# Kernel tuning notes

Hardware: AMD Instinct MI355X
Metric: run time of the kernel (lower is better)

## Reference

```python
import jax, jax.numpy as jnp
import numpy as np
import math

B, L, D, H = 4, 1024, 512, 8
TAU = 0.1
LN_EPS = 1e-5


def _attn(xq, xk, xv, wq, bq, wk, bk, wv, bv, wo, bo, energy=None, threshold=None):
    Bq, Lq, Dm = xq.shape
    Dh = Dm // H
    Q = (xq @ wq.T + bq).reshape(Bq, Lq, H, Dh)
    K = (xk @ wk.T + bk).reshape(Bq, -1, H, Dh)
    V = (xv @ wv.T + bv).reshape(Bq, -1, H, Dh)
    sc = jnp.einsum('bqhd,bkhd->bhqk', Q, K) / jnp.sqrt(jnp.float32(Dh))
    if energy is not None:
        # mask keys whose mean |energy| over channels is below threshold
        mask = jnp.abs(energy).mean(-1)[:, None, None, :] > threshold  # (B,1,1,Lk)
        sc = jnp.where(mask, sc, -jnp.inf)
    w = jnp.nan_to_num(jax.nn.softmax(sc, axis=-1))  # nan->0 for fully-masked rows
    o = jnp.einsum('bhqk,bkhd->bqhd', w, V).reshape(Bq, Lq, Dm)
    return o @ wo.T + bo


def _ln(x, w, b):
    m = x.mean(-1, keepdims=True)
    v = x.var(-1, keepdims=True)
    return (x - m) / jnp.sqrt(v + LN_EPS) * w + b


def _mlp(x, w1, b1, w2, b2):
    h = jax.nn.gelu(x @ w1.T + b1, approximate=False)  # torch nn.GELU default = exact
    return h @ w2.T + b2


def setup_inputs():
    key = jax.random.key(0)
    ks = list(jax.random.split(key, 64))

    def nxt():
        return ks.pop(0)

    def w(shape, scale=0.02):
        return jax.random.normal(nxt(), shape, dtype=jnp.float32) * scale

    inp = {
        'LL': jax.random.normal(nxt(), (B, D, L), dtype=jnp.float32),
        'LH': jax.random.normal(nxt(), (B, D, L), dtype=jnp.float32),
        'raw_tau': jnp.float32(math.log(TAU / (1.0 - TAU))),
    }
    for p in ('llA', 'lhA', 'crA'):
        for nm in ('q', 'k', 'v', 'o'):
            inp[f'{p}_w{nm}'] = w((D, D))
            inp[f'{p}_b{nm}'] = jnp.zeros((D,), jnp.float32)
    for p in ('mlp_ll', 'mlp_lh'):
        inp[f'{p}_w1'] = w((4 * D, D))
        inp[f'{p}_b1'] = jnp.zeros((4 * D,), jnp.float32)
        inp[f'{p}_w2'] = w((D, 4 * D))
        inp[f'{p}_b2'] = jnp.zeros((D,), jnp.float32)
    inp['n1_w'] = jnp.ones((D,), jnp.float32)
    inp['n1_b'] = jnp.zeros((D,), jnp.float32)
    inp['n2_w'] = jnp.ones((D,), jnp.float32)
    inp['n2_b'] = jnp.zeros((D,), jnp.float32)
    return inp


def reference(LL, LH, raw_tau,
              llA_wq, llA_bq, llA_wk, llA_bk, llA_wv, llA_bv, llA_wo, llA_bo,
              lhA_wq, lhA_bq, lhA_wk, lhA_bk, lhA_wv, lhA_bv, lhA_wo, lhA_bo,
              crA_wq, crA_bq, crA_wk, crA_bk, crA_wv, crA_bv, crA_wo, crA_bo,
              mlp_ll_w1, mlp_ll_b1, mlp_ll_w2, mlp_ll_b2,
              mlp_lh_w1, mlp_lh_b1, mlp_lh_w2, mlp_lh_b2,
              n1_w, n1_b, n2_w, n2_b):
    tau = jax.nn.sigmoid(raw_tau)
    ll_s = jnp.transpose(LL, (0, 2, 1))  # (B,L,D)
    lh_s = jnp.transpose(LH, (0, 2, 1))
    ll_o = _attn(ll_s, ll_s, ll_s, llA_wq, llA_bq, llA_wk, llA_bk, llA_wv, llA_bv, llA_wo, llA_bo)
    lh_o = _attn(lh_s, lh_s, lh_s, lhA_wq, lhA_bq, lhA_wk, lhA_bk, lhA_wv, lhA_bv, lhA_wo, lhA_bo,
                 energy=lh_s, threshold=tau)
    cr_o = _attn(ll_o, lh_o, lh_o, crA_wq, crA_bq, crA_wk, crA_bk, crA_wv, crA_bv, crA_wo, crA_bo)
    ll_f = _ln(ll_s + ll_o + cr_o, n1_w, n1_b)
    ll_f = _mlp(ll_f, mlp_ll_w1, mlp_ll_b1, mlp_ll_w2, mlp_ll_b2) + ll_f
    lh_f = _ln(lh_s + lh_o, n2_w, n2_b)
    lh_f = _mlp(lh_f, mlp_lh_w1, mlp_lh_b1, mlp_lh_w2, mlp_lh_b2) + lh_f
    return (jnp.transpose(ll_f, (0, 2, 1)), jnp.transpose(lh_f, (0, 2, 1)))
```

## Files before the change

kernel.cpp:

```cpp
#include <hip/hip_runtime.h>
#include <hip/hip_bf16.h>
#include <stdint.h>

typedef unsigned short u16;
typedef __bf16 bf16_t;
typedef bf16_t bf16x8 __attribute__((ext_vector_type(8)));
typedef float f32x4 __attribute__((ext_vector_type(4)));

#define DEV static __device__ __forceinline__

DEV u16 f2b(float f) {
    __hip_bfloat16 h = __float2bfloat16(f);
    return __builtin_bit_cast(u16, h);
}

DEV bf16x8 ld_frag(const u16* p) {
    uint4 u = *reinterpret_cast<const uint4*>(p);
    return __builtin_bit_cast(bf16x8, u);
}

DEV void gl_lds16(const u16* g, u16* l) {
    __builtin_amdgcn_global_load_lds(
        (const __attribute__((address_space(1))) void*)(uintptr_t)g,
        (__attribute__((address_space(3))) void*)(unsigned int)(uintptr_t)l,
        16, 0, 0);
}

struct ConvEnt { const float* s; u16* d; int n; };
struct ConvArgs { ConvEnt e[16]; };

__global__ __launch_bounds__(256) void k_conv(ConvArgs a) {
    const ConvEnt en = a.e[blockIdx.y];
    int i = (blockIdx.x * 256 + threadIdx.x) * 4;
    if (i >= en.n) return;
    const float4 f = *reinterpret_cast<const float4*>(en.s + i);
    unsigned r0 = (unsigned)f2b(f.x) | ((unsigned)f2b(f.y) << 16);
    unsigned r1 = (unsigned)f2b(f.z) | ((unsigned)f2b(f.w) << 16);
    uint2 rr; rr.x = r0; rr.y = r1;
    *reinterpret_cast<uint2*>(en.d + i) = rr;
}

struct CpyEnt { const float* s; float* d; };
struct CpyArgs { CpyEnt e[8]; };

__global__ __launch_bounds__(256) void k_cpyf(CpyArgs a) {
    const CpyEnt en = a.e[blockIdx.y];
    int i = blockIdx.x * 256 + threadIdx.x;
    en.d[i] = en.s[i];
}

__global__ __launch_bounds__(256) void k_tin(const float* __restrict__ in,
                                             float* __restrict__ of, u16* __restrict__ ob) {
    __shared__ float t[32][33];
    int b = blockIdx.z, l0 = blockIdx.x * 32, d0 = blockIdx.y * 32;
    int tx = threadIdx.x, ty = threadIdx.y;
#pragma unroll
    for (int j = 0; j < 4; ++j) {
        int d = d0 + ty + j * 8;
        t[ty + j * 8][tx] = in[((size_t)b * 512 + d) * 1024 + l0 + tx];
    }
    __syncthreads();
#pragma unroll
    for (int j = 0; j < 4; ++j) {
        int l = l0 + ty + j * 8;
        float v = t[tx][ty + j * 8];
        size_t o = ((size_t)b * 1024 + l) * 512 + d0 + tx;
        of[o] = v;
        ob[o] = f2b(v);
    }
}

__global__ __launch_bounds__(256) void k_tout(const float* __restrict__ in, float* __restrict__ out) {
    __shared__ float t[32][33];
    int b = blockIdx.z, l0 = blockIdx.x * 32, d0 = blockIdx.y * 32;
    int tx = threadIdx.x, ty = threadIdx.y;
#pragma unroll
    for (int j = 0; j < 4; ++j) {
        int l = l0 + ty + j * 8;
        t[ty + j * 8][tx] = in[((size_t)b * 1024 + l) * 512 + d0 + tx];
    }
    __syncthreads();
#pragma unroll
    for (int j = 0; j < 4; ++j) {
        int d = d0 + ty + j * 8;
        out[((size_t)b * 512 + d) * 1024 + l0 + tx] = t[tx][ty + j * 8];
    }
}

__global__ __launch_bounds__(256) void k_mask(const float* __restrict__ lh_s,
                                              const float* __restrict__ raw_tau,
                                              float* __restrict__ kbias) {
    int row = blockIdx.x * 4 + (threadIdx.x >> 6);
    int lane = threadIdx.x & 63;
    const float* p = lh_s + (size_t)row * 512 + lane * 8;
    float s = 0.f;
#pragma unroll
    for (int j = 0; j < 8; ++j) s += fabsf(p[j]);
#pragma unroll
    for (int m = 32; m >= 1; m >>= 1) s += __shfl_xor(s, m, 64);
    float tau = 1.f / (1.f + expf(-raw_tau[0]));
    if (lane == 0) kbias[row] = (s * (1.f / 512.f) > tau) ? 0.f : -3.0e38f;
}

__global__ __launch_bounds__(256) void k_ln(const float* __restrict__ a, const float* __restrict__ b,
                                            const float* __restrict__ c, const float* __restrict__ w,
                                            const float* __restrict__ bi,
                                            float* __restrict__ of, u16* __restrict__ ob) {
    int row = blockIdx.x * 4 + (threadIdx.x >> 6);
    int lane = threadIdx.x & 63;
    size_t base = (size_t)row * 512 + lane * 8;
    float x[8];
#pragma unroll
    for (int j = 0; j < 8; ++j) {
        float v = a[base + j] + b[base + j];
        if (c) v += c[base + j];
        x[j] = v;
    }
    float s = 0.f, s2 = 0.f;
#pragma unroll
    for (int j = 0; j < 8; ++j) { s += x[j]; s2 += x[j] * x[j]; }
#pragma unroll
    for (int m = 32; m >= 1; m >>= 1) { s += __shfl_xor(s, m, 64); s2 += __shfl_xor(s2, m, 64); }
    float mean = s * (1.f / 512.f);
    float var = s2 * (1.f / 512.f) - mean * mean;
    float rs = rsqrtf(var + 1e-5f);
#pragma unroll
    for (int j = 0; j < 8; ++j) {
        float y = (x[j] - mean) * rs * w[lane * 8 + j] + bi[lane * 8 + j];
        of[base + j] = y;
        ob[base + j] = f2b(y);
    }
}

template <int BM, int BN, int GELU_ACT, int OUTF, int OUTB, int RES, int PACK>
__global__ __launch_bounds__(256) void k_gemm(const u16* __restrict__ A, const u16* __restrict__ W,
                                              const float* __restrict__ bias,
                                              const float* __restrict__ res,
                                              float* __restrict__ Cf, u16* __restrict__ Cb,
                                              u16* __restrict__ Qp, u16* __restrict__ Kp,
                                              u16* __restrict__ Vt, int kB, int vB,
                                              int M, int N, int K) {
    constexpr int BK = 64;
    __shared__ alignas(16) u16 Al[2][BM * BK];
    __shared__ alignas(16) u16 Wl[2][BN * BK];
    const int t = threadIdx.x, w = t >> 6, l = t & 63;
    const int m0 = blockIdx.x * BM, n0 = blockIdx.y * BN;
    constexpr int FM = BM / 32, FN = BN / 32;
    const int wr = w >> 1, wc = w & 1;
    const int lq = l & 15, lg = l >> 4;
    f32x4 acc[FM][FN] = {};

    const int srow = l >> 3, scol = (l & 7) * 8;
    auto stage = [&](int kcol, int buf) {
#pragma unroll
        for (int i = 0; i < BM / 32; ++i)
            gl_lds16(A + (size_t)(m0 + i * 32 + w * 8 + srow) * K + kcol + scol, &Al[buf][(i * 32 + w * 8) * BK]);
#pragma unroll
        for (int i = 0; i < BN / 32; ++i)
            gl_lds16(W + (size_t)(n0 + i * 32 + w * 8 + srow) * K + kcol + scol, &Wl[buf][(i * 32 + w * 8) * BK]);
    };

    stage(0, 0);
    const int KT = K / BK;
    for (int kt = 0; kt < KT; ++kt) {
        const int cur = kt & 1;
        __syncthreads();
        if (kt + 1 < KT) stage((kt + 1) * BK, cur ^ 1);
#pragma unroll
        for (int s = 0; s < 2; ++s) {
            bf16x8 af[FM], bw[FN];
#pragma unroll
            for (int i = 0; i < FM; ++i)
                af[i] = ld_frag(&Al[cur][(wr * (BM / 2) + i * 16 + lq) * BK + s * 32 + lg * 8]);
#pragma unroll
            for (int j = 0; j < FN; ++j)
                bw[j] = ld_frag(&Wl[cur][(wc * (BN / 2) + j * 16 + lq) * BK + s * 32 + lg * 8]);
#pragma unroll
            for (int i = 0; i < FM; ++i)
#pragma unroll
                for (int j = 0; j < FN; ++j)
                    acc[i][j] = __builtin_amdgcn_mfma_f32_16x16x32_bf16(af[i], bw[j], acc[i][j], 0, 0, 0);
        }
    }
#pragma unroll
    for (int i = 0; i < FM; ++i) {
#pragma unroll
        for (int j = 0; j < FN; ++j) {
            const int n = n0 + wc * (BN / 2) + j * 16 + lq;
            const float bn = bias[n];
#pragma unroll
            for (int r = 0; r < 4; ++r) {
                const int m = m0 + wr * (BM / 2) + i * 16 + lg * 4 + r;
                float v = acc[i][j][r] + bn;
                if (GELU_ACT) v = 0.5f * v * (1.f + erff(v * 0.70710678118654752f));
                if (PACK) {
                    const int bb = m >> 10, ll_ = m & 1023;
                    if (n >= vB) {
                        const int d = n - vB;
                        Vt[((size_t)(bb * 8 + (d >> 6)) * 64 + (d & 63)) * 1024 + ll_] = f2b(v);
                    } else if (n >= kB) {
                        const int d = n - kB;
                        Kp[((size_t)(bb * 8 + (d >> 6)) * 1024 + ll_) * 64 + (d & 63)] = f2b(v);
                    } else {
                        Qp[((size_t)(bb * 8 + (n >> 6)) * 1024 + ll_) * 64 + (n & 63)] = f2b(v * 0.125f);
                    }
                } else {
                    size_t o = (size_t)m * N + n;
                    if (RES) v += res[o];
                    if (OUTF) Cf[o] = v;
                    if (OUTB) Cb[o] = f2b(v);
                }
            }
        }
    }
}

template <int HAS_BIAS>
__global__ __launch_bounds__(256) void k_attn(const u16* __restrict__ Qp, const u16* __restrict__ Kp,
                                              const u16* __restrict__ Vtp, u16* __restrict__ O,
                                              const float* __restrict__ kbias) {
    constexpr int L = 1024;
    __shared__ alignas(16) u16 Kl[2][64 * 64];
    __shared__ alignas(16) u16 Vl[2][64 * 64];
    __shared__ alignas(16) u16 Pl[64 * 72];
    const int t = threadIdx.x, w = t >> 6, l = t & 63;
    const int q0 = blockIdx.x * 64;
    const int h = blockIdx.y, b = blockIdx.z, bh = b * 8 + h;
    const int lq = l & 15, lg = l >> 4;

    bf16x8 qa0, qa1;
    {
        const u16* qp = Qp + ((size_t)bh * L + q0 + w * 16 + lq) * 64 + lg * 8;
        qa0 = ld_frag(qp);
        qa1 = ld_frag(qp + 32);
    }

    const int r0 = w * 16 + (l >> 3), r1 = r0 + 8, c = l & 7;
    const u16* Ksrc0 = Kp + (size_t)bh * L * 64 + (size_t)r0 * 64 + ((c ^ (r0 & 7)) * 8);
    const u16* Ksrc1 = Kp + (size_t)bh * L * 64 + (size_t)r1 * 64 + ((c ^ (r1 & 7)) * 8);
    const u16* Vsrc0 = Vtp + (size_t)bh * 64 * L + (size_t)r0 * L + ((c ^ (r0 & 7)) * 8);
    const u16* Vsrc1 = Vtp + (size_t)bh * 64 * L + (size_t)r1 * L + ((c ^ (r1 & 7)) * 8);

    auto stage = [&](int k0, int buf) {
        gl_lds16(Ksrc0 + (size_t)k0 * 64, &Kl[buf][(w * 16) * 64]);
        gl_lds16(Ksrc1 + (size_t)k0 * 64, &Kl[buf][(w * 16 + 8) * 64]);
        gl_lds16(Vsrc0 + k0, &Vl[buf][(w * 16) * 64]);
        gl_lds16(Vsrc1 + k0, &Vl[buf][(w * 16 + 8) * 64]);
    };

    int addrA[4][2];
#pragma unroll
    for (int f = 0; f < 4; ++f) {
        int row = f * 16 + lq;
#pragma unroll
        for (int s = 0; s < 2; ++s) addrA[f][s] = row * 64 + (((s * 4 + lg) ^ (row & 7)) * 8);
    }
    const int paddr0 = (w * 16 + lq) * 72 + lg * 8;

    f32x4 oacc[4] = {};
    float lrow[4] = {0.f, 0.f, 0.f, 0.f};

    stage(0, 0);
    for (int kt = 0; kt < 16; ++kt) {
        const int cur = kt & 1;
        __syncthreads();
        if (kt + 1 < 16) stage((kt + 1) * 64, cur ^ 1);

        f32x4 sc4[4];
#pragma unroll
        for (int f = 0; f < 4; ++f) {
            f32x4 a = {};
            a = __builtin_amdgcn_mfma_f32_16x16x32_bf16(qa0, ld_frag(&Kl[cur][addrA[f][0]]), a, 0, 0, 0);
            a = __builtin_amdgcn_mfma_f32_16x16x32_bf16(qa1, ld_frag(&Kl[cur][addrA[f][1]]), a, 0, 0, 0);
            sc4[f] = a;
        }
#pragma unroll
        for (int f = 0; f < 4; ++f) {
            float bv = 0.f;
            if (HAS_BIAS) bv = kbias[(size_t)b * L + kt * 64 + f * 16 + lq];
#pragma unroll
            for (int r = 0; r < 4; ++r) {
                float pv = __expf(HAS_BIAS ? (sc4[f][r] + bv) : sc4[f][r]);
                lrow[r] += pv;
                Pl[(w * 16 + lg * 4 + r) * 72 + f * 16 + lq] = f2b(pv);
            }
        }
        bf16x8 pa0 = ld_frag(&Pl[paddr0]);
        bf16x8 pa1 = ld_frag(&Pl[paddr0 + 32]);
#pragma unroll
        for (int db = 0; db < 4; ++db) {
            oacc[db] = __builtin_amdgcn_mfma_f32_16x16x32_bf16(pa0, ld_frag(&Vl[cur][addrA[db][0]]), oacc[db], 0, 0, 0);
            oacc[db] = __builtin_amdgcn_mfma_f32_16x16x32_bf16(pa1, ld_frag(&Vl[cur][addrA[db][1]]), oacc[db], 0, 0, 0);
        }
    }
#pragma unroll
    for (int r = 0; r < 4; ++r) {
        float v = lrow[r];
#pragma unroll
        for (int msk = 8; msk >= 1; msk >>= 1) v += __shfl_xor(v, msk, 16);
        lrow[r] = v;
    }
#pragma unroll
    for (int db = 0; db < 4; ++db) {
#pragma unroll
        for (int r = 0; r < 4; ++r) {
            float denom = lrow[r];
            float v = (denom > 0.f) ? oacc[db][r] / denom : 0.f;
            O[((size_t)b * L + q0 + w * 16 + lg * 4 + r) * 512 + h * 64 + db * 16 + lq] = f2b(v);
        }
    }
}

extern "C" void kernel_launch(void* const* d_in, const int* in_sizes, int n_in,
                              void* d_out, int out_size, void* d_ws, size_t ws_size,
                              hipStream_t stream) {
    const int M = 4096, D = 512, DFF = 2048, Bz = 4, Lz = 1024, Hz = 8;
    const float* LL = (const float*)d_in[0];
    const float* LH = (const float*)d_in[1];
    const float* raw_tau = (const float*)d_in[2];
    auto F = [&](int i) { return (const float*)d_in[i]; };
    const int BIG = 1 << 28;

    char* p = (char*)d_ws;
    auto alloc = [&](size_t bytes) { void* r = (void*)p; p += (bytes + 255) & ~(size_t)255; return r; };
    const size_t MDf = (size_t)M * D * 4, MDb = (size_t)M * D * 2;
    float* ll_s_f = (float*)alloc(MDf);
    float* lh_s_f = (float*)alloc(MDf);
    u16* ll_s_b = (u16*)alloc(MDb);
    u16* lh_s_b = (u16*)alloc(MDb);
    u16* Qp = (u16*)alloc(MDb);
    u16* Kp = (u16*)alloc(MDb);
    u16* Vt = (u16*)alloc(MDb);
    u16* Cxb = (u16*)alloc(MDb);
    float* ll_o_f = (float*)alloc(MDf);
    u16* ll_o_b = (u16*)alloc(MDb);
    float* lh_o_f = (float*)alloc(MDf);
    u16* lh_o_b = (u16*)alloc(MDb);
    float* cr_o_f = (float*)alloc(MDf);
    float* ln_f = (float*)alloc(MDf);
    u16* ln_b = (u16*)alloc(MDb);
    u16* hb = (u16*)alloc((size_t)M * DFF * 2);
    float* yf = (float*)alloc(MDf);
    float* kbias = (float*)alloc(4096 * 4);
    float* bqkv_ll = (float*)alloc(1536 * 4);
    float* bqkv_lh = (float*)alloc(1536 * 4);
    float* bkv_cr = (float*)alloc(1024 * 4);
    const size_t WDD = (size_t)262144;
    u16* wqkv_ll = (u16*)alloc(3 * WDD * 2);
    u16* wqkv_lh = (u16*)alloc(3 * WDD * 2);
    u16* wkv_cr = (u16*)alloc(2 * WDD * 2);
    u16* wq_cr = (u16*)alloc(WDD * 2);
    u16* wo_ll = (u16*)alloc(WDD * 2);
    u16* wo_lh = (u16*)alloc(WDD * 2);
    u16* wo_cr = (u16*)alloc(WDD * 2);
    u16* wm[4];
    for (int i = 0; i < 4; ++i) wm[i] = (u16*)alloc((size_t)1048576 * 2);

    ConvArgs ca;
    ca.e[0] = {F(3), wqkv_ll, (int)WDD};
    ca.e[1] = {F(5), wqkv_ll + WDD, (int)WDD};
    ca.e[2] = {F(7), wqkv_ll + 2 * WDD, (int)WDD};
    ca.e[3] = {F(11), wqkv_lh, (int)WDD};
    ca.e[4] = {F(13), wqkv_lh + WDD, (int)WDD};
    ca.e[5] = {F(15), wqkv_lh + 2 * WDD, (int)WDD};
    ca.e[6] = {F(19), wq_cr, (int)WDD};
    ca.e[7] = {F(21), wkv_cr, (int)WDD};
    ca.e[8] = {F(23), wkv_cr + WDD, (int)WDD};
    ca.e[9] = {F(9), wo_ll, (int)WDD};
    ca.e[10] = {F(17), wo_lh, (int)WDD};
    ca.e[11] = {F(25), wo_cr, (int)WDD};
    ca.e[12] = {F(27), wm[0], 1048576};
    ca.e[13] = {F(29), wm[1], 1048576};
    ca.e[14] = {F(31), wm[2], 1048576};
    ca.e[15] = {F(33), wm[3], 1048576};
    k_conv<<<dim3(1024, 16), 256, 0, stream>>>(ca);

    CpyArgs cp;
    cp.e[0] = {F(4), bqkv_ll};
    cp.e[1] = {F(6), bqkv_ll + 512};
    cp.e[2] = {F(8), bqkv_ll + 1024};
    cp.e[3] = {F(12), bqkv_lh};
    cp.e[4] = {F(14), bqkv_lh + 512};
    cp.e[5] = {F(16), bqkv_lh + 1024};
    cp.e[6] = {F(22), bkv_cr};
    cp.e[7] = {F(24), bkv_cr + 512};
    k_cpyf<<<dim3(2, 8), 256, 0, stream>>>(cp);

    k_tin<<<dim3(32, 16, Bz), dim3(32, 8), 0, stream>>>(LL, ll_s_f, ll_s_b);
    k_tin<<<dim3(32, 16, Bz), dim3(32, 8), 0, stream>>>(LH, lh_s_f, lh_s_b);
    k_mask<<<dim3(1024), 256, 0, stream>>>(lh_s_f, raw_tau, kbias);

    dim3 g64(M / 64, D / 64);
    dim3 gattn(Lz / 64, Hz, Bz);

    k_gemm<128, 128, 0, 0, 0, 0, 1><<<dim3(M / 128, 1536 / 128), 256, 0, stream>>>(
        ll_s_b, wqkv_ll, bqkv_ll, nullptr, nullptr, nullptr, Qp, Kp, Vt, 512, 1024, M, 1536, D);
    k_attn<0><<<gattn, 256, 0, stream>>>(Qp, Kp, Vt, Cxb, nullptr);
    k_gemm<64, 64, 0, 1, 1, 0, 0><<<g64, 256, 0, stream>>>(
        Cxb, wo_ll, F(10), nullptr, ll_o_f, ll_o_b, nullptr, nullptr, nullptr, 0, 0, M, D, D);

    k_gemm<128, 128, 0, 0, 0, 0, 1><<<dim3(M / 128, 1536 / 128), 256, 0, stream>>>(
        lh_s_b, wqkv_lh, bqkv_lh, nullptr, nullptr, nullptr, Qp, Kp, Vt, 512, 1024, M, 1536, D);
    k_attn<1><<<gattn, 256, 0, stream>>>(Qp, Kp, Vt, Cxb, kbias);
    k_gemm<64, 64, 0, 1, 1, 0, 0><<<g64, 256, 0, stream>>>(
        Cxb, wo_lh, F(18), nullptr, lh_o_f, lh_o_b, nullptr, nullptr, nullptr, 0, 0, M, D, D);

    k_gemm<64, 64, 0, 0, 0, 0, 1><<<g64, 256, 0, stream>>>(
        ll_o_b, wq_cr, F(20), nullptr, nullptr, nullptr, Qp, Kp, Vt, BIG, BIG, M, D, D);
    k_gemm<64, 64, 0, 0, 0, 0, 1><<<dim3(M / 64, 1024 / 64), 256, 0, stream>>>(
        lh_o_b, wkv_cr, bkv_cr, nullptr, nullptr, nullptr, Qp, Kp, Vt, 0, 512, M, 1024, D);
    k_attn<0><<<gattn, 256, 0, stream>>>(Qp, Kp, Vt, Cxb, nullptr);
    k_gemm<64, 64, 0, 1, 0, 0, 0><<<g64, 256, 0, stream>>>(
        Cxb, wo_cr, F(26), nullptr, cr_o_f, nullptr, nullptr, nullptr, nullptr, 0, 0, M, D, D);

    k_ln<<<dim3(1024), 256, 0, stream>>>(ll_s_f, ll_o_f, cr_o_f, F(35), F(36), ln_f, ln_b);
    k_gemm<128, 128, 1, 0, 1, 0, 0><<<dim3(M / 128, DFF / 128), 256, 0, stream>>>(
        ln_b, wm[0], F(28), nullptr, nullptr, hb, nullptr, nullptr, nullptr, 0, 0, M, DFF, D);
    k_gemm<64, 64, 0, 1, 0, 1, 0><<<g64, 256, 0, stream>>>(
        hb, wm[1], F(30), ln_f, yf, nullptr, nullptr, nullptr, nullptr, 0, 0, M, D, DFF);
    k_tout<<<dim3(32, 16, Bz), dim3(32, 8), 0, stream>>>(yf, (float*)d_out);

    k_ln<<<dim3(1024), 256, 0, stream>>>(lh_s_f, lh_o_f, nullptr, F(37), F(38), ln_f, ln_b);
    k_gemm<128, 128, 1, 0, 1, 0, 0><<<dim3(M / 128, DFF / 128), 256, 0, stream>>>(
        ln_b, wm[2], F(32), nullptr, nullptr, hb, nullptr, nullptr, nullptr, 0, 0, M, DFF, D);
    k_gemm<64, 64, 0, 1, 0, 1, 0><<<g64, 256, 0, stream>>>(
        hb, wm[3], F(34), ln_f, yf, nullptr, nullptr, nullptr, nullptr, 0, 0, M, D, DFF);
    k_tout<<<dim3(32, 16, Bz), dim3(32, 8), 0, stream>>>(yf, (float*)d_out + (size_t)M * D);
}
```

Measured before the change: 318.8 us.

## Batch independent GEMMs and attentions into grouped launches with reordered schedule

Replaces the templated GEMM with a descriptor-driven grouped GEMM, so several independent matmuls (LL and LH QKV projections, output projections, cross-attention projections together with the LH MLP up-projection) run in one launch over a shared block range. The two self-attentions run as one launch by stacking the batches, and the input and output transposes are merged the same way. The LH branch's LayerNorm and MLP are moved earlier so they overlap with the cross-attention work. This cuts launch count and fills the GPU better for small grids. The cost is runtime flags instead of compile-time template branches in the GEMM epilogue, extra scratch buffers, and a uniform tile size for mixed shapes.

```diff
diff --git a/kernel.cpp b/kernel.cpp
--- a/kernel.cpp
+++ b/kernel.cpp
@@ -49,10 +49,15 @@
     en.d[i] = en.s[i];
 }
 
-__global__ __launch_bounds__(256) void k_tin(const float* __restrict__ in,
-                                             float* __restrict__ of, u16* __restrict__ ob) {
+__global__ __launch_bounds__(256) void k_tin(const float* __restrict__ LL, const float* __restrict__ LH,
+                                             float* __restrict__ llf, u16* __restrict__ llb,
+                                             float* __restrict__ lhf, u16* __restrict__ lhb) {
     __shared__ float t[32][33];
-    int b = blockIdx.z, l0 = blockIdx.x * 32, d0 = blockIdx.y * 32;
+    int z = blockIdx.z, b = z & 3;
+    const float* in = (z < 4) ? LL : LH;
+    float* of = (z < 4) ? llf : lhf;
+    u16* ob = (z < 4) ? llb : lhb;
+    int l0 = blockIdx.x * 32, d0 = blockIdx.y * 32;
     int tx = threadIdx.x, ty = threadIdx.y;
 #pragma unroll
     for (int j = 0; j < 4; ++j) {
@@ -70,9 +75,13 @@
     }
 }
 
-__global__ __launch_bounds__(256) void k_tout(const float* __restrict__ in, float* __restrict__ out) {
+__global__ __launch_bounds__(256) void k_tout(const float* __restrict__ y0, const float* __restrict__ y1,
+                                              float* __restrict__ out) {
     __shared__ float t[32][33];
-    int b = blockIdx.z, l0 = blockIdx.x * 32, d0 = blockIdx.y * 32;
+    int z = blockIdx.z, b = z & 3;
+    const float* in = (z < 4) ? y0 : y1;
+    float* o = out + ((z < 4) ? 0 : (size_t)4096 * 512);
+    int l0 = blockIdx.x * 32, d0 = blockIdx.y * 32;
     int tx = threadIdx.x, ty = threadIdx.y;
 #pragma unroll
     for (int j = 0; j < 4; ++j) {
@@ -83,7 +92,7 @@
 #pragma unroll
     for (int j = 0; j < 4; ++j) {
         int d = d0 + ty + j * 8;
-        out[((size_t)b * 512 + d) * 1024 + l0 + tx] = t[tx][ty + j * 8];
+        o[((size_t)b * 512 + d) * 1024 + l0 + tx] = t[tx][ty + j * 8];
     }
 }
 
@@ -132,19 +141,33 @@
     }
 }
 
-template <int BM, int BN, int GELU_ACT, int OUTF, int OUTB, int RES, int PACK>
-__global__ __launch_bounds__(256) void k_gemm(const u16* __restrict__ A, const u16* __restrict__ W,
-                                              const float* __restrict__ bias,
-                                              const float* __restrict__ res,
-                                              float* __restrict__ Cf, u16* __restrict__ Cb,
-                                              u16* __restrict__ Qp, u16* __restrict__ Kp,
-                                              u16* __restrict__ Vt, int kB, int vB,
-                                              int M, int N, int K) {
+struct GDesc {
+    const u16* A; const u16* W; const float* bias; const float* res;
+    float* Cf; u16* Cb; u16* Qp; u16* Kp; u16* Vt;
+    int kB, vB;
+    int N, K;
+    int gelu, outf, outb, isres, pack;
+    int nbx, blk0;
+};
+struct GArgs { GDesc d[3]; int nd; };
+
+template <int BM, int BN>
+__global__ __launch_bounds__(256) void k_bgemm(GArgs ga) {
     constexpr int BK = 64;
     __shared__ alignas(16) u16 Al[2][BM * BK];
     __shared__ alignas(16) u16 Wl[2][BN * BK];
+    int di = 0;
+    if (ga.nd > 1 && (int)blockIdx.x >= ga.d[1].blk0) di = 1;
+    if (ga.nd > 2 && (int)blockIdx.x >= ga.d[2].blk0) di = 2;
+    GDesc g;
+    if (di == 0) g = ga.d[0];
+    else if (di == 1) g = ga.d[1];
+    else g = ga.d[2];
+    const int rel = blockIdx.x - g.blk0;
+    const int m0 = (rel % g.nbx) * BM, n0 = (rel / g.nbx) * BN;
+    const int K = g.K, N = g.N;
+
     const int t = threadIdx.x, w = t >> 6, l = t & 63;
-    const int m0 = blockIdx.x * BM, n0 = blockIdx.y * BN;
     constexpr int FM = BM / 32, FN = BN / 32;
     const int wr = w >> 1, wc = w & 1;
     const int lq = l & 15, lg = l >> 4;
@@ -154,10 +177,10 @@
     auto stage = [&](int kcol, int buf) {
 #pragma unroll
         for (int i = 0; i < BM / 32; ++i)
-            gl_lds16(A + (size_t)(m0 + i * 32 + w * 8 + srow) * K + kcol + scol, &Al[buf][(i * 32 + w * 8) * BK]);
+            gl_lds16(g.A + (size_t)(m0 + i * 32 + w * 8 + srow) * K + kcol + scol, &Al[buf][(i * 32 + w * 8) * BK]);
 #pragma unroll
         for (int i = 0; i < BN / 32; ++i)
-            gl_lds16(W + (size_t)(n0 + i * 32 + w * 8 + srow) * K + kcol + scol, &Wl[buf][(i * 32 + w * 8) * BK]);
+            gl_lds16(g.W + (size_t)(n0 + i * 32 + w * 8 + srow) * K + kcol + scol, &Wl[buf][(i * 32 + w * 8) * BK]);
     };
 
     stage(0, 0);
@@ -187,35 +210,34 @@
 #pragma unroll
         for (int j = 0; j < FN; ++j) {
             const int n = n0 + wc * (BN / 2) + j * 16 + lq;
-            const float bn = bias[n];
+            const float bn = g.bias[n];
 #pragma unroll
             for (int r = 0; r < 4; ++r) {
                 const int m = m0 + wr * (BM / 2) + i * 16 + lg * 4 + r;
                 float v = acc[i][j][r] + bn;
-                if (GELU_ACT) v = 0.5f * v * (1.f + erff(v * 0.70710678118654752f));
-                if (PACK) {
+                if (g.gelu) v = 0.5f * v * (1.f + erff(v * 0.70710678118654752f));
+                if (g.pack) {
                     const int bb = m >> 10, ll_ = m & 1023;
-                    if (n >= vB) {
-                        const int d = n - vB;
-                        Vt[((size_t)(bb * 8 + (d >> 6)) * 64 + (d & 63)) * 1024 + ll_] = f2b(v);
-                    } else if (n >= kB) {
-                        const int d = n - kB;
-                        Kp[((size_t)(bb * 8 + (d >> 6)) * 1024 + ll_) * 64 + (d & 63)] = f2b(v);
+                    if (n >= g.vB) {
+                        const int d = n - g.vB;
+                        g.Vt[((size_t)(bb * 8 + (d >> 6)) * 64 + (d & 63)) * 1024 + ll_] = f2b(v);
+                    } else if (n >= g.kB) {
+                        const int d = n - g.kB;
+                        g.Kp[((size_t)(bb * 8 + (d >> 6)) * 1024 + ll_) * 64 + (d & 63)] = f2b(v);
                     } else {
-                        Qp[((size_t)(bb * 8 + (n >> 6)) * 1024 + ll_) * 64 + (n & 63)] = f2b(v * 0.125f);
+                        g.Qp[((size_t)(bb * 8 + (n >> 6)) * 1024 + ll_) * 64 + (n & 63)] = f2b(v * 0.125f);
                     }
                 } else {
                     size_t o = (size_t)m * N + n;
-                    if (RES) v += res[o];
-                    if (OUTF) Cf[o] = v;
-                    if (OUTB) Cb[o] = f2b(v);
+                    if (g.isres) v += g.res[o];
+                    if (g.outf) g.Cf[o] = v;
+                    if (g.outb) g.Cb[o] = f2b(v);
                 }
             }
         }
     }
 }
 
-template <int HAS_BIAS>
 __global__ __launch_bounds__(256) void k_attn(const u16* __restrict__ Qp, const u16* __restrict__ Kp,
                                               const u16* __restrict__ Vtp, u16* __restrict__ O,
                                               const float* __restrict__ kbias) {
@@ -225,8 +247,9 @@
     __shared__ alignas(16) u16 Pl[64 * 72];
     const int t = threadIdx.x, w = t >> 6, l = t & 63;
     const int q0 = blockIdx.x * 64;
-    const int h = blockIdx.y, b = blockIdx.z, bh = b * 8 + h;
+    const int h = blockIdx.y, bz = blockIdx.z, bh = bz * 8 + h;
     const int lq = l & 15, lg = l >> 4;
+    const float* kb = (kbias != nullptr && bz >= 4) ? (kbias + (size_t)(bz - 4) * L) : nullptr;
 
     bf16x8 qa0, qa1;
     {
@@ -276,11 +299,10 @@
         }
 #pragma unroll
         for (int f = 0; f < 4; ++f) {
-            float bv = 0.f;
-            if (HAS_BIAS) bv = kbias[(size_t)b * L + kt * 64 + f * 16 + lq];
+            float bv = kb ? kb[kt * 64 + f * 16 + lq] : 0.f;
 #pragma unroll
             for (int r = 0; r < 4; ++r) {
-                float pv = __expf(HAS_BIAS ? (sc4[f][r] + bv) : sc4[f][r]);
+                float pv = __expf(sc4[f][r] + bv);
                 lrow[r] += pv;
                 Pl[(w * 16 + lg * 4 + r) * 72 + f * 16 + lq] = f2b(pv);
             }
@@ -306,7 +328,7 @@
         for (int r = 0; r < 4; ++r) {
             float denom = lrow[r];
             float v = (denom > 0.f) ? oacc[db][r] / denom : 0.f;
-            O[((size_t)b * L + q0 + w * 16 + lg * 4 + r) * 512 + h * 64 + db * 16 + lq] = f2b(v);
+            O[((size_t)bz * L + q0 + w * 16 + lg * 4 + r) * 512 + h * 64 + db * 16 + lq] = f2b(v);
         }
     }
 }
@@ -328,19 +350,21 @@
     float* lh_s_f = (float*)alloc(MDf);
     u16* ll_s_b = (u16*)alloc(MDb);
     u16* lh_s_b = (u16*)alloc(MDb);
-    u16* Qp = (u16*)alloc(MDb);
-    u16* Kp = (u16*)alloc(MDb);
-    u16* Vt = (u16*)alloc(MDb);
-    u16* Cxb = (u16*)alloc(MDb);
+    u16* Qp = (u16*)alloc(2 * MDb);
+    u16* Kp = (u16*)alloc(2 * MDb);
+    u16* Vt = (u16*)alloc(2 * MDb);
+    u16* Cxb = (u16*)alloc(2 * MDb);
     float* ll_o_f = (float*)alloc(MDf);
     u16* ll_o_b = (u16*)alloc(MDb);
     float* lh_o_f = (float*)alloc(MDf);
     u16* lh_o_b = (u16*)alloc(MDb);
     float* cr_o_f = (float*)alloc(MDf);
-    float* ln_f = (float*)alloc(MDf);
+    float* ln_f_ll = (float*)alloc(MDf);
+    float* ln_f_lh = (float*)alloc(MDf);
     u16* ln_b = (u16*)alloc(MDb);
     u16* hb = (u16*)alloc((size_t)M * DFF * 2);
-    float* yf = (float*)alloc(MDf);
+    float* yf_ll = (float*)alloc(MDf);
+    float* yf_lh = (float*)alloc(MDf);
     float* kbias = (float*)alloc(4096 * 4);
     float* bqkv_ll = (float*)alloc(1536 * 4);
     float* bqkv_lh = (float*)alloc(1536 * 4);
@@ -355,6 +379,8 @@
     u16* wo_cr = (u16*)alloc(WDD * 2);
     u16* wm[4];
     for (int i = 0; i < 4; ++i) wm[i] = (u16*)alloc((size_t)1048576 * 2);
+
+    const size_t SET = (size_t)4 * 8 * 1024 * 64;
 
     ConvArgs ca;
     ca.e[0] = {F(3), wqkv_ll, (int)WDD};
@@ -386,44 +412,68 @@
     cp.e[7] = {F(24), bkv_cr + 512};
     k_cpyf<<<dim3(2, 8), 256, 0, stream>>>(cp);
 
-    k_tin<<<dim3(32, 16, Bz), dim3(32, 8), 0, stream>>>(LL, ll_s_f, ll_s_b);
-    k_tin<<<dim3(32, 16, Bz), dim3(32, 8), 0, stream>>>(LH, lh_s_f, lh_s_b);
+    k_tin<<<dim3(32, 16, 8), dim3(32, 8), 0, stream>>>(LL, LH, ll_s_f, ll_s_b, lh_s_f, lh_s_b);
     k_mask<<<dim3(1024), 256, 0, stream>>>(lh_s_f, raw_tau, kbias);
 
-    dim3 g64(M / 64, D / 64);
-    dim3 gattn(Lz / 64, Hz, Bz);
-
-    k_gemm<128, 128, 0, 0, 0, 0, 1><<<dim3(M / 128, 1536 / 128), 256, 0, stream>>>(
-        ll_s_b, wqkv_ll, bqkv_ll, nullptr, nullptr, nullptr, Qp, Kp, Vt, 512, 1024, M, 1536, D);
-    k_attn<0><<<gattn, 256, 0, stream>>>(Qp, Kp, Vt, Cxb, nullptr);
-    k_gemm<64, 64, 0, 1, 1, 0, 0><<<g64, 256, 0, stream>>>(
-        Cxb, wo_ll, F(10), nullptr, ll_o_f, ll_o_b, nullptr, nullptr, nullptr, 0, 0, M, D, D);
-
-    k_gemm<128, 128, 0, 0, 0, 0, 1><<<dim3(M / 128, 1536 / 128), 256, 0, stream>>>(
-        lh_s_b, wqkv_lh, bqkv_lh, nullptr, nullptr, nullptr, Qp, Kp, Vt, 512, 1024, M, 1536, D);
-    k_attn<1><<<gattn, 256, 0, stream>>>(Qp, Kp, Vt, Cxb, kbias);
-    k_gemm<64, 64, 0, 1, 1, 0, 0><<<g64, 256, 0, stream>>>(
-        Cxb, wo_lh, F(18), nullptr, lh_o_f, lh_o_b, nullptr, nullptr, nullptr, 0, 0, M, D, D);
-
-    k_gemm<64, 64, 0, 0, 0, 0, 1><<<g64, 256, 0, stream>>>(
-        ll_o_b, wq_cr, F(20), nullptr, nullptr, nullptr, Qp, Kp, Vt, BIG, BIG, M, D, D);
-    k_gemm<64, 64, 0, 0, 0, 0, 1><<<dim3(M / 64, 1024 / 64), 256, 0, stream>>>(
-        lh_o_b, wkv_cr, bkv_cr, nullptr, nullptr, nullptr, Qp, Kp, Vt, 0, 512, M, 1024, D);
-    k_attn<0><<<gattn, 256, 0, stream>>>(Qp, Kp, Vt, Cxb, nullptr);
-    k_gemm<64, 64, 0, 1, 0, 0, 0><<<g64, 256, 0, stream>>>(
-        Cxb, wo_cr, F(26), nullptr, cr_o_f, nullptr, nullptr, nullptr, nullptr, 0, 0, M, D, D);
-
-    k_ln<<<dim3(1024), 256, 0, stream>>>(ll_s_f, ll_o_f, cr_o_f, F(35), F(36), ln_f, ln_b);
-    k_gemm<128, 128, 1, 0, 1, 0, 0><<<dim3(M / 128, DFF / 128), 256, 0, stream>>>(
-        ln_b, wm[0], F(28), nullptr, nullptr, hb, nullptr, nullptr, nullptr, 0, 0, M, DFF, D);
-    k_gemm<64, 64, 0, 1, 0, 1, 0><<<g64, 256, 0, stream>>>(
-        hb, wm[1], F(30), ln_f, yf, nullptr, nullptr, nullptr, nullptr, 0, 0, M, D, DFF);
-    k_tout<<<dim3(32, 16, Bz), dim3(32, 8), 0, stream>>>(yf, (float*)d_out);
-
-    k_ln<<<dim3(1024), 256, 0, stream>>>(lh_s_f, lh_o_f, nullptr, F(37), F(38), ln_f, ln_b);
-    k_gemm<128, 128, 1, 0, 1, 0, 0><<<dim3(M / 128, DFF / 128), 256, 0, stream>>>(
-        ln_b, wm[2], F(32), nullptr, nullptr, hb, nullptr, nullptr, nullptr, 0, 0, M, DFF, D);
-    k_gemm<64, 64, 0, 1, 0, 1, 0><<<g64, 256, 0, stream>>>(
-        hb, wm[3], F(34), ln_f, yf, nullptr, nullptr, nullptr, nullptr, 0, 0, M, D, DFF);
-    k_tout<<<dim3(32, 16, Bz), dim3(32, 8), 0, stream>>>(yf, (float*)d_out + (size_t)M * D);
-}
+    auto desc = [&](const u16* A, const u16* W, const float* bias, int N, int K,
+                    int nbx, int blk0) {
+        GDesc g = {};
+        g.A = A; g.W = W; g.bias = bias; g.N = N; g.K = K; g.nbx = nbx; g.blk0 = blk0;
+        g.kB = BIG; g.vB = BIG;
+        return g;
+    };
+
+    {
+        GArgs ga; ga.nd = 2;
+        ga.d[0] = desc(ll_s_b, wqkv_ll, bqkv_ll, 1536, 512, 32, 0);
+        ga.d[0].pack = 1; ga.d[0].kB = 512; ga.d[0].vB = 1024;
+        ga.d[0].Qp = Qp; ga.d[0].Kp = Kp; ga.d[0].Vt = Vt;
+        ga.d[1] = desc(lh_s_b, wqkv_lh, bqkv_lh, 1536, 512, 32, 384);
+        ga.d[1].pack = 1; ga.d[1].kB = 512; ga.d[1].vB = 1024;
+        ga.d[1].Qp = Qp + SET; ga.d[1].Kp = Kp + SET; ga.d[1].Vt = Vt + SET;
+        k_bgemm<128, 128><<<dim3(768), 256, 0, stream>>>(ga);
+    }
+    k_attn<<<dim3(16, 8, 8), 256, 0, stream>>>(Qp, Kp, Vt, Cxb, kbias);
+    {
+        GArgs ga; ga.nd = 2;
+        ga.d[0] = desc(Cxb, wo_ll, F(10), 512, 512, 64, 0);
+        ga.d[0].outf = 1; ga.d[0].outb = 1; ga.d[0].Cf = ll_o_f; ga.d[0].Cb = ll_o_b;
+        ga.d[1] = desc(Cxb + SET, wo_lh, F(18), 512, 512, 64, 512);
+        ga.d[1].outf = 1; ga.d[1].outb = 1; ga.d[1].Cf = lh_o_f; ga.d[1].Cb = lh_o_b;
+        k_bgemm<64, 64><<<dim3(1024), 256, 0, stream>>>(ga);
+    }
+    k_ln<<<dim3(1024), 256, 0, stream>>>(lh_s_f, lh_o_f, nullptr, F(37), F(38), ln_f_lh, ln_b);
+    {
+        GArgs ga; ga.nd = 3;
+        ga.d[0] = desc(ll_o_b, wq_cr, F(20), 512, 512, 32, 0);
+        ga.d[0].pack = 1; ga.d[0].kB = BIG; ga.d[0].vB = BIG; ga.d[0].Qp = Qp;
+        ga.d[1] = desc(lh_o_b, wkv_cr, bkv_cr, 1024, 512, 32, 256);
+        ga.d[1].pack = 1; ga.d[1].kB = 0; ga.d[1].vB = 512; ga.d[1].Kp = Kp; ga.d[1].Vt = Vt;
+        ga.d[2] = desc(ln_b, wm[2], F(32), 2048, 512, 32, 768);
+        ga.d[2].gelu = 1; ga.d[2].outb = 1; ga.d[2].Cb = hb;
+        k_bgemm<128, 64><<<dim3(1792), 256, 0, stream>>>(ga);
+    }
+    k_attn<<<dim3(16, 8, 4), 256, 0, stream>>>(Qp, Kp, Vt, Cxb, nullptr);
+    {
+        GArgs ga; ga.nd = 2;
+        ga.d[0] = desc(Cxb, wo_cr, F(26), 512, 512, 64, 0);
+        ga.d[0].outf = 1; ga.d[0].Cf = cr_o_f;
+        ga.d[1] = desc(hb, wm[3], F(34), 512, 2048, 64, 512);
+        ga.d[1].outf = 1; ga.d[1].isres = 1; ga.d[1].Cf = yf_lh; ga.d[1].res = ln_f_lh;
+        k_bgemm<64, 64><<<dim3(1024), 256, 0, stream>>>(ga);
+    }
+    k_ln<<<dim3(1024), 256, 0, stream>>>(ll_s_f, ll_o_f, cr_o_f, F(35), F(36), ln_f_ll, ln_b);
+    {
+        GArgs ga; ga.nd = 1;
+        ga.d[0] = desc(ln_b, wm[0], F(28), 2048, 512, 32, 0);
+        ga.d[0].gelu = 1; ga.d[0].outb = 1; ga.d[0].Cb = hb;
+        k_bgemm<128, 128><<<dim3(512), 256, 0, stream>>>(ga);
+    }
+    {
+        GArgs ga; ga.nd = 1;
+        ga.d[0] = desc(hb, wm[1], F(30), 512, 2048, 64, 0);
+        ga.d[0].outf = 1; ga.d[0].isres = 1; ga.d[0].Cf = yf_ll; ga.d[0].res = ln_f_ll;
+        k_bgemm<64, 64><<<dim3(512), 256, 0, stream>>>(ga);
+    }
+    k_tout<<<dim3(32, 16, 8), dim3(32, 8), 0, stream>>>(yf_ll, yf_lh, (float*)d_out);
+}
```

Result: slower. 329.0 us (+3.2%).
